# Kernel optimization log

Hardware: AMD Instinct MI355X
Metric: run time of the kernel (lower is better)

The kernel has to match this reference:

```python
import jax, jax.numpy as jnp
import numpy as np

D_MODEL = 1024
HEAD = 16
D_K = D_MODEL // HEAD


def setup_inputs() -> dict:
    key = jax.random.key(0)
    ks = jax.random.split(key, 11)
    B, S = 2, 2048
    scale = 1.0 / np.sqrt(D_MODEL)
    inp = {
        "q": jax.random.normal(ks[0], (B, S, D_MODEL), dtype=jnp.float32),
        "k": jax.random.normal(ks[1], (B, S, D_MODEL), dtype=jnp.float32),
        "v": jax.random.normal(ks[2], (B, S, D_MODEL), dtype=jnp.float32),
        "wq": jax.random.normal(ks[3], (D_MODEL, D_MODEL), dtype=jnp.float32) * scale,
        "bq": jnp.zeros((D_MODEL,), dtype=jnp.float32),
        "wk": jax.random.normal(ks[4], (D_MODEL, D_MODEL), dtype=jnp.float32) * scale,
        "bk": jnp.zeros((D_MODEL,), dtype=jnp.float32),
        "wv": jax.random.normal(ks[5], (D_MODEL, D_MODEL), dtype=jnp.float32) * scale,
        "bv": jnp.zeros((D_MODEL,), dtype=jnp.float32),
        "wo": jax.random.normal(ks[6], (D_MODEL, D_MODEL), dtype=jnp.float32) * scale,
        "bo": jnp.zeros((D_MODEL,), dtype=jnp.float32),
    }
    return inp


def reference(q, k, v, wq, bq, wk, bk, wv, bv, wo, bo):
    B, S, _ = q.shape
    # linear projections, split into heads: [B, H, S, Dk]
    def proj(x, w, b):
        y = x @ w.T + b
        return y.reshape(B, -1, HEAD, D_K).transpose(0, 2, 1, 3)

    qh, kh, vh = proj(q, wq, bq), proj(k, wk, bk), proj(v, wv, bv)
    # scaled dot-product attention (dropout = identity in eval)
    scores = jnp.einsum("bhqd,bhkd->bhqk", qh, kh) / jnp.sqrt(jnp.float32(D_K))
    probs = jax.nn.softmax(scores, axis=-1)
    ctx = jnp.einsum("bhqk,bhkd->bhqd", probs, vh)
    concat = ctx.transpose(0, 2, 1, 3).reshape(B, S, D_MODEL)
    return concat @ wo.T + bo
```

## Files before the change

### kernel.cpp

```cpp
#include <hip/hip_runtime.h>
#include <stdint.h>

#define S_LEN 2048
#define NH 16
#define DK 64
#define DMODEL 1024

typedef __attribute__((ext_vector_type(8))) _Float16 half8;
typedef __attribute__((ext_vector_type(4))) _Float16 half4;
typedef __attribute__((ext_vector_type(4))) float f32x4;
typedef __attribute__((ext_vector_type(16))) float f32x16;

#define OFF_QX   0u
#define OFF_KX   4194304u
#define OFF_VX   8388608u
#define OFF_WQ   12582912u
#define OFF_WK   13631488u
#define OFF_WV   14680064u
#define OFF_WO   15728640u
#define OFF_QH   16777216u
#define OFF_KH   20971520u
#define OFF_VH   25165824u
#define OFF_CTX  29360128u

#define LOG2E 1.44269504088896340736f
#define SOFT_M 10.0f

__device__ __forceinline__ f32x4 mfma_f16(half8 a, half8 b, f32x4 c) {
  return __builtin_amdgcn_mfma_f32_16x16x32_f16(a, b, c, 0, 0, 0);
}
__device__ __forceinline__ f32x16 mfma32(half8 a, half8 b, f32x16 c) {
  return __builtin_amdgcn_mfma_f32_32x32x16_f16(a, b, c, 0, 0, 0);
}

__device__ __forceinline__ void gload16(const void* g, void* l) {
  __builtin_amdgcn_global_load_lds(
      (const __attribute__((address_space(1))) uint32_t*)g,
      (__attribute__((address_space(3))) uint32_t*)l, 16, 0, 0);
}

__global__ void cast_f32_f16(const float* __restrict__ q, const float* __restrict__ k,
                             const float* __restrict__ v, const float* __restrict__ wq,
                             const float* __restrict__ wk, const float* __restrict__ wv,
                             const float* __restrict__ wo, _Float16* __restrict__ ws16) {
  const int seg = blockIdx.y;
  const float* src;
  unsigned n, doff;
  switch (seg) {
    case 0: src = q;  n = 4194304u; doff = OFF_QX; break;
    case 1: src = k;  n = 4194304u; doff = OFF_KX; break;
    case 2: src = v;  n = 4194304u; doff = OFF_VX; break;
    case 3: src = wq; n = 1048576u; doff = OFF_WQ; break;
    case 4: src = wk; n = 1048576u; doff = OFF_WK; break;
    case 5: src = wv; n = 1048576u; doff = OFF_WV; break;
    default: src = wo; n = 1048576u; doff = OFF_WO; break;
  }
  unsigned i = (blockIdx.x * 256u + threadIdx.x) * 4u;
  if (i >= n) return;
  float4 f = *(const float4*)(src + i);
  half4 h;
  h.x = (_Float16)f.x; h.y = (_Float16)f.y; h.z = (_Float16)f.z; h.w = (_Float16)f.w;
  *(half4*)(ws16 + doff + i) = h;
}

__global__ __launch_bounds__(256, 3) void gemm_qkv(
    _Float16* __restrict__ ws16, const float* __restrict__ bq,
    const float* __restrict__ bk, const float* __restrict__ bv) {
  const int t = threadIdx.x;
  const int w = t >> 6, lane = t & 63, l16 = lane & 15, quad = lane >> 4;
  const int wx = w & 1, wy = w >> 1;
  const int bx = blockIdx.x;
  const int which = bx >> 3;
  const int n0 = (bx & 7) * 128;
  const int m0 = blockIdx.y * 128;

  const _Float16* A  = ws16 + (which == 0 ? OFF_QX : which == 1 ? OFF_KX : OFF_VX);
  const _Float16* Bt = ws16 + (which == 0 ? OFF_WQ : which == 1 ? OFF_WK : OFF_WV);
  const float* bias  = (which == 0) ? bq : (which == 1) ? bk : bv;
  _Float16* dst      = ws16 + (which == 0 ? OFF_QH : which == 1 ? OFF_KH : OFF_VH);
  const float scale  = (which == 0) ? 0.125f * LOG2E : 1.0f;

  __shared__ _Float16 smem[2][128][64];
  _Float16 (*As)[64] = smem[0];
  _Float16 (*Bs)[64] = smem[1];

  f32x4 zero = {0.f, 0.f, 0.f, 0.f};
  f32x4 acc[4][4];
#pragma unroll
  for (int i = 0; i < 4; i++)
#pragma unroll
    for (int j = 0; j < 4; j++) acc[i][j] = zero;

  const int lr = lane >> 3;
  const int gch = (lane & 7) ^ lr;
  const _Float16* gA[4];
  const _Float16* gB[4];
  _Float16* lA[4];
  _Float16* lB[4];
#pragma unroll
  for (int j = 0; j < 4; j++) {
    int n = w * 4 + j;
    gA[j] = A + (size_t)(m0 + n * 8 + lr) * DMODEL + gch * 8;
    gB[j] = Bt + (size_t)(n0 + n * 8 + lr) * DMODEL + gch * 8;
    lA[j] = &As[n * 8][0];
    lB[j] = &Bs[n * 8][0];
  }
  const int xr = l16 & 7;
  const int c0 = (quad ^ xr) * 8;
  const int c1 = ((4 + quad) ^ xr) * 8;

  for (int k0 = 0; k0 < DMODEL; k0 += 64) {
    __syncthreads();
#pragma unroll
    for (int j = 0; j < 4; j++) {
      gload16(gA[j] + k0, lA[j]);
      gload16(gB[j] + k0, lB[j]);
    }
    __syncthreads();

    half8 af[2][4], bf[2][4];
#pragma unroll
    for (int i = 0; i < 4; i++) {
      af[0][i] = *(const half8*)&As[wy * 64 + i * 16 + l16][c0];
      af[1][i] = *(const half8*)&As[wy * 64 + i * 16 + l16][c1];
      bf[0][i] = *(const half8*)&Bs[wx * 64 + i * 16 + l16][c0];
      bf[1][i] = *(const half8*)&Bs[wx * 64 + i * 16 + l16][c1];
    }
#pragma unroll
    for (int s = 0; s < 2; s++)
#pragma unroll
      for (int i = 0; i < 4; i++)
#pragma unroll
        for (int j = 0; j < 4; j++)
          acc[i][j] = mfma_f16(af[s][i], bf[s][j], acc[i][j]);
  }

  if (which == 2) {
#pragma unroll
    for (int j = 0; j < 4; j++) {
      int n = n0 + wx * 64 + j * 16 + l16;
      float bn = bias[n];
      int h = n >> 6, d = n & 63;
#pragma unroll
      for (int i = 0; i < 4; i++) {
        int m = m0 + wy * 64 + i * 16 + quad * 4;
        int b = m >> 11, s = m & 2047;
        half4 hv;
#pragma unroll
        for (int r = 0; r < 4; r++) hv[r] = (_Float16)(acc[i][j][r] + bn);
        *(half4*)(dst + ((size_t)(b * NH + h) * DK + d) * S_LEN + s) = hv;
      }
    }
  } else {
    _Float16* Cs = &smem[0][0][0];
    __syncthreads();
#pragma unroll
    for (int j = 0; j < 4; j++) {
      int n = wx * 64 + j * 16 + l16;
      float bn = bias[n0 + n];
      int cl = n >> 3, nb = n & 7;
#pragma unroll
      for (int i = 0; i < 4; i++) {
#pragma unroll
        for (int r = 0; r < 4; r++) {
          int m = wy * 64 + i * 16 + quad * 4 + r;
          int cp = cl ^ (m & 15);
          Cs[m * 128 + cp * 8 + nb] = (_Float16)((acc[i][j][r] + bn) * scale);
        }
      }
    }
    __syncthreads();
#pragma unroll
    for (int p = 0; p < 8; p++) {
      int row = (t >> 4) + p * 16;
      int cl = t & 15;
      int cp = cl ^ (row & 15);
      half8 v = *(const half8*)&Cs[row * 128 + cp * 8];
      int m = m0 + row;
      int b = m >> 11, s = m & 2047;
      int ng = n0 + cl * 8;
      int h = ng >> 6, d = ng & 63;
      *(half8*)(dst + ((size_t)(b * NH + h) * S_LEN + s) * DK + d) = v;
    }
  }
}

__global__ __launch_bounds__(256, 2) void attn(_Float16* __restrict__ ws16) {
  const int t = threadIdx.x;
  const int w = t >> 6, lane = t & 63;
  const int l32 = lane & 31, hi = lane >> 5;
  const int wg = blockIdx.y * 16 + blockIdx.x;
  const int xcd = wg & 7, ix = wg >> 3;
  const int bh = (xcd << 2) | (ix >> 4);
  const int q0 = (ix & 15) * 128 + w * 32;

  const _Float16* Qh  = ws16 + OFF_QH + (size_t)bh * S_LEN * DK;
  const _Float16* Kh  = ws16 + OFF_KH + (size_t)bh * S_LEN * DK;
  const _Float16* VhT = ws16 + OFF_VH + (size_t)bh * DK * S_LEN;
  _Float16* ctx = ws16 + OFF_CTX;

  __shared__ _Float16 Ks[2][64][64];
  __shared__ _Float16 Vt[2][64][64];
  __shared__ _Float16 Ps[4][32][68];

  half8 qb[4];
#pragma unroll
  for (int c = 0; c < 4; c++)
    qb[c] = *(const half8*)(Qh + (size_t)(q0 + l32) * DK + c * 16 + hi * 8);

  f32x16 o_acc[2];
#pragma unroll
  for (int dt = 0; dt < 2; dt++)
#pragma unroll
    for (int r = 0; r < 16; r++) o_acc[dt][r] = 0.f;
  float lsum = 0.f;

  f32x16 minit;
#pragma unroll
  for (int r = 0; r < 16; r++) minit[r] = -SOFT_M;

  const int lr = lane >> 3;
  const int gch = (lane & 7) ^ lr;
  const _Float16* gk0 = Kh + (size_t)(w * 8 + lr) * DK + gch * 8;
  const _Float16* gk1 = Kh + (size_t)(32 + w * 8 + lr) * DK + gch * 8;
  const _Float16* gv0 = VhT + (size_t)(w * 8 + lr) * S_LEN + gch * 8;
  const _Float16* gv1 = VhT + (size_t)(32 + w * 8 + lr) * S_LEN + gch * 8;

  const int sw = l32 & 7;

  gload16(gk0, &Ks[0][w * 8][0]);
  gload16(gk1, &Ks[0][32 + w * 8][0]);
  gload16(gv0, &Vt[0][w * 8][0]);
  gload16(gv1, &Vt[0][32 + w * 8][0]);
  __syncthreads();

  for (int kt2 = 0; kt2 < 16; kt2++) {
#pragma unroll
    for (int h = 0; h < 2; h++) {
      const int kt = kt2 * 2 + h;
      const int cur = h;

      if (kt < 31) {
        const int kb = (kt + 1) * 64;
        gload16(gk0 + (size_t)kb * DK, &Ks[cur ^ 1][w * 8][0]);
        gload16(gk1 + (size_t)kb * DK, &Ks[cur ^ 1][32 + w * 8][0]);
        gload16(gv0 + kb, &Vt[cur ^ 1][w * 8][0]);
        gload16(gv1 + kb, &Vt[cur ^ 1][32 + w * 8][0]);
      }
      __builtin_amdgcn_sched_barrier(0);

#pragma unroll
      for (int ktile = 0; ktile < 2; ktile++) {
        const int krow = ktile * 32 + l32;
        f32x16 sc = minit;
#pragma unroll
        for (int c = 0; c < 4; c++) {
          half8 af = *(const half8*)&Ks[cur][krow][((2 * c + hi) ^ sw) * 8];
          sc = mfma32(af, qb[c], sc);
        }
#pragma unroll
        for (int g = 0; g < 4; g++) {
          half4 pk;
#pragma unroll
          for (int u = 0; u < 4; u++) {
            float p = __builtin_amdgcn_exp2f(sc[g * 4 + u]);
            lsum += p;
            pk[u] = (_Float16)p;
          }
          *(half4*)&Ps[w][l32][ktile * 32 + g * 8 + hi * 4] = pk;
        }
      }

      half8 ap[4];
#pragma unroll
      for (int kc = 0; kc < 4; kc++)
        ap[kc] = *(const half8*)&Ps[w][l32][kc * 16 + hi * 8];
#pragma unroll
      for (int dt = 0; dt < 2; dt++) {
        const int drow = dt * 32 + l32;
        f32x16 c = o_acc[dt];
#pragma unroll
        for (int kc = 0; kc < 4; kc++) {
          half8 bf = *(const half8*)&Vt[cur][drow][((2 * kc + hi) ^ sw) * 8];
          c = mfma32(ap[kc], bf, c);
        }
        o_acc[dt] = c;
      }

      __syncthreads();
    }
  }

  lsum += __shfl_xor(lsum, 32);
  float inv = 1.0f / lsum;

  const int b = bh >> 4, hh = bh & 15;
#pragma unroll
  for (int r = 0; r < 16; r++) {
    int qloc = (r & 3) + 8 * (r >> 2) + 4 * hi;
    float iv = __shfl(inv, qloc);
    int sq = q0 + qloc;
    size_t base = ((size_t)(b * S_LEN + sq)) * DMODEL + hh * DK + l32;
    ctx[base] = (_Float16)(o_acc[0][r] * iv);
    ctx[base + 32] = (_Float16)(o_acc[1][r] * iv);
  }
}

__global__ __launch_bounds__(256, 3) void gemm_out(
    const _Float16* __restrict__ ws16, const float* __restrict__ bo,
    float* __restrict__ out) {
  const int t = threadIdx.x;
  const int w = t >> 6, lane = t & 63, l16 = lane & 15, quad = lane >> 4;
  const int wx = w & 1, wy = w >> 1;
  const int n0 = blockIdx.x * 128;
  const int m0 = blockIdx.y * 128;

  const _Float16* A = ws16 + OFF_CTX;
  const _Float16* Bt = ws16 + OFF_WO;

  __shared__ _Float16 As[128][64];
  __shared__ _Float16 Bs[128][64];

  f32x4 zero = {0.f, 0.f, 0.f, 0.f};
  f32x4 acc[4][4];
#pragma unroll
  for (int i = 0; i < 4; i++)
#pragma unroll
    for (int j = 0; j < 4; j++) acc[i][j] = zero;

  const int lr = lane >> 3;
  const int gch = (lane & 7) ^ lr;
  const _Float16* gA[4];
  const _Float16* gB[4];
  _Float16* lA[4];
  _Float16* lB[4];
#pragma unroll
  for (int j = 0; j < 4; j++) {
    int n = w * 4 + j;
    gA[j] = A + (size_t)(m0 + n * 8 + lr) * DMODEL + gch * 8;
    gB[j] = Bt + (size_t)(n0 + n * 8 + lr) * DMODEL + gch * 8;
    lA[j] = &As[n * 8][0];
    lB[j] = &Bs[n * 8][0];
  }
  const int xr = l16 & 7;
  const int c0 = (quad ^ xr) * 8;
  const int c1 = ((4 + quad) ^ xr) * 8;

  for (int k0 = 0; k0 < DMODEL; k0 += 64) {
    __syncthreads();
#pragma unroll
    for (int j = 0; j < 4; j++) {
      gload16(gA[j] + k0, lA[j]);
      gload16(gB[j] + k0, lB[j]);
    }
    __syncthreads();

    half8 af[2][4], bf[2][4];
#pragma unroll
    for (int i = 0; i < 4; i++) {
      af[0][i] = *(const half8*)&As[wy * 64 + i * 16 + l16][c0];
      af[1][i] = *(const half8*)&As[wy * 64 + i * 16 + l16][c1];
      bf[0][i] = *(const half8*)&Bs[wx * 64 + i * 16 + l16][c0];
      bf[1][i] = *(const half8*)&Bs[wx * 64 + i * 16 + l16][c1];
    }
#pragma unroll
    for (int s = 0; s < 2; s++)
#pragma unroll
      for (int i = 0; i < 4; i++)
#pragma unroll
        for (int j = 0; j < 4; j++)
          acc[i][j] = mfma_f16(af[s][i], bf[s][j], acc[i][j]);
  }

#pragma unroll
  for (int j = 0; j < 4; j++) {
    int n = n0 + wx * 64 + j * 16 + l16;
    float bn = bo[n];
#pragma unroll
    for (int i = 0; i < 4; i++) {
#pragma unroll
      for (int r = 0; r < 4; r++) {
        int m = m0 + wy * 64 + i * 16 + quad * 4 + r;
        out[(size_t)m * DMODEL + n] = acc[i][j][r] + bn;
      }
    }
  }
}

extern "C" void kernel_launch(void* const* d_in, const int* in_sizes, int n_in,
                              void* d_out, int out_size, void* d_ws, size_t ws_size,
                              hipStream_t stream) {
  const float* q  = (const float*)d_in[0];
  const float* k  = (const float*)d_in[1];
  const float* v  = (const float*)d_in[2];
  const float* wq = (const float*)d_in[3];
  const float* bq = (const float*)d_in[4];
  const float* wk = (const float*)d_in[5];
  const float* bk = (const float*)d_in[6];
  const float* wv = (const float*)d_in[7];
  const float* bv = (const float*)d_in[8];
  const float* wo = (const float*)d_in[9];
  const float* bo = (const float*)d_in[10];
  float* out = (float*)d_out;
  _Float16* ws16 = (_Float16*)d_ws;

  cast_f32_f16<<<dim3(4096, 7), 256, 0, stream>>>(q, k, v, wq, wk, wv, wo, ws16);
  gemm_qkv<<<dim3(24, 32), 256, 0, stream>>>(ws16, bq, bk, bv);
  attn<<<dim3(16, 32), 256, 0, stream>>>(ws16);
  gemm_out<<<dim3(8, 32), 256, 0, stream>>>(ws16, bo, out);
}
```

Before: 227.7 us.

## Keep attention probabilities in registers via permlane32 swap instead of LDS round-trip

```diff
diff --git a/kernel.cpp b/kernel.cpp
--- a/kernel.cpp
+++ b/kernel.cpp
@@ -10,6 +10,7 @@
 typedef __attribute__((ext_vector_type(4))) _Float16 half4;
 typedef __attribute__((ext_vector_type(4))) float f32x4;
 typedef __attribute__((ext_vector_type(16))) float f32x16;
+typedef __attribute__((ext_vector_type(4))) uint32_t u32x4;
 
 #define OFF_QX   0u
 #define OFF_KX   4194304u
@@ -37,6 +38,11 @@
   __builtin_amdgcn_global_load_lds(
       (const __attribute__((address_space(1))) uint32_t*)g,
       (__attribute__((address_space(3))) uint32_t*)l, 16, 0, 0);
+}
+
+__device__ __forceinline__ uint32_t pkrtz(float a, float b) {
+  auto pk2 = __builtin_amdgcn_cvt_pkrtz(a, b);
+  return __builtin_bit_cast(uint32_t, pk2);
 }
 
 __global__ void cast_f32_f16(const float* __restrict__ q, const float* __restrict__ k,
@@ -201,7 +207,6 @@
 
   __shared__ _Float16 Ks[2][64][64];
   __shared__ _Float16 Vt[2][64][64];
-  __shared__ _Float16 Ps[4][32][68];
 
   half8 qb[4];
 #pragma unroll
@@ -213,7 +218,7 @@
   for (int dt = 0; dt < 2; dt++)
 #pragma unroll
     for (int r = 0; r < 16; r++) o_acc[dt][r] = 0.f;
-  float lsum = 0.f;
+  float ls[4] = {0.f, 0.f, 0.f, 0.f};
 
   f32x16 minit;
 #pragma unroll
@@ -253,44 +258,51 @@
       for (int ktile = 0; ktile < 2; ktile++) {
         const int krow = ktile * 32 + l32;
         f32x16 sc = minit;
+        __builtin_amdgcn_s_setprio(1);
 #pragma unroll
         for (int c = 0; c < 4; c++) {
           half8 af = *(const half8*)&Ks[cur][krow][((2 * c + hi) ^ sw) * 8];
           sc = mfma32(af, qb[c], sc);
         }
-#pragma unroll
-        for (int g = 0; g < 4; g++) {
-          half4 pk;
-#pragma unroll
-          for (int u = 0; u < 4; u++) {
-            float p = __builtin_amdgcn_exp2f(sc[g * 4 + u]);
-            lsum += p;
-            pk[u] = (_Float16)p;
-          }
-          *(half4*)&Ps[w][l32][ktile * 32 + g * 8 + hi * 4] = pk;
+        __builtin_amdgcn_s_setprio(0);
+
+        float pv[16];
+#pragma unroll
+        for (int i = 0; i < 16; i++) {
+          pv[i] = __builtin_amdgcn_exp2f(sc[i]);
+          ls[i & 3] += pv[i];
         }
+        uint32_t wd[8];
+#pragma unroll
+        for (int j = 0; j < 8; j++) {
+          wd[j] = pkrtz(pv[2 * j], pv[2 * j + 1]);
+        }
+        asm("v_permlane32_swap_b32 %0, %1" : "+v"(wd[0]), "+v"(wd[2]));
+        asm("v_permlane32_swap_b32 %0, %1" : "+v"(wd[1]), "+v"(wd[3]));
+        asm("v_permlane32_swap_b32 %0, %1" : "+v"(wd[4]), "+v"(wd[6]));
+        asm("v_permlane32_swap_b32 %0, %1" : "+v"(wd[5]), "+v"(wd[7]));
+        u32x4 aw0 = {wd[0], wd[1], wd[2], wd[3]};
+        u32x4 aw1 = {wd[4], wd[5], wd[6], wd[7]};
+        half8 ap0 = __builtin_bit_cast(half8, aw0);
+        half8 ap1 = __builtin_bit_cast(half8, aw1);
+
+        __builtin_amdgcn_s_setprio(1);
+#pragma unroll
+        for (int dt = 0; dt < 2; dt++) {
+          const int drow = dt * 32 + l32;
+          f32x16 c = o_acc[dt];
+          c = mfma32(ap0, *(const half8*)&Vt[cur][drow][((2 * (ktile * 2 + 0) + hi) ^ sw) * 8], c);
+          c = mfma32(ap1, *(const half8*)&Vt[cur][drow][((2 * (ktile * 2 + 1) + hi) ^ sw) * 8], c);
+          o_acc[dt] = c;
+        }
+        __builtin_amdgcn_s_setprio(0);
       }
 
-      half8 ap[4];
-#pragma unroll
-      for (int kc = 0; kc < 4; kc++)
-        ap[kc] = *(const half8*)&Ps[w][l32][kc * 16 + hi * 8];
-#pragma unroll
-      for (int dt = 0; dt < 2; dt++) {
-        const int drow = dt * 32 + l32;
-        f32x16 c = o_acc[dt];
-#pragma unroll
-        for (int kc = 0; kc < 4; kc++) {
-          half8 bf = *(const half8*)&Vt[cur][drow][((2 * kc + hi) ^ sw) * 8];
-          c = mfma32(ap[kc], bf, c);
-        }
-        o_acc[dt] = c;
-      }
-
       __syncthreads();
     }
   }
 
+  float lsum = (ls[0] + ls[1]) + (ls[2] + ls[3]);
   lsum += __shfl_xor(lsum, 32);
   float inv = 1.0f / lsum;
 
```

Measured after the change: 224.3 us. Within noise of the previous version (-1.5%).
